# Optimization experiments

Measured on AMD Instinct MI355X. Metric: run time of the kernel, lower is better.

## Reference

```python
import jax, jax.numpy as jnp
import numpy as np
import math

D_MODEL = 1024
NHEAD = 16
D_K = D_MODEL // NHEAD
NUM_LAYERS = 4
D_FF = 4096
SEQ = 2048
BATCH = 1
EPS = 1e-5


def _layer_norm(x, g, b):
    mu = jnp.mean(x, axis=-1, keepdims=True)
    var = jnp.mean((x - mu) ** 2, axis=-1, keepdims=True)
    return (x - mu) * jax.lax.rsqrt(var + EPS) * g + b


def setup_inputs() -> dict:
    key = jax.random.key(0)
    ks = jax.random.split(key, 16)
    s = 0.02
    L, D, F = NUM_LAYERS, D_MODEL, D_FF
    inp = {
        "x": jax.random.normal(ks[0], (BATCH, SEQ, D), dtype=jnp.float32),
        "wq": jax.random.normal(ks[1], (L, D, D), dtype=jnp.float32) * s,
        "bq": jnp.zeros((L, D), dtype=jnp.float32),
        "wk": jax.random.normal(ks[2], (L, D, D), dtype=jnp.float32) * s,
        "bk": jnp.zeros((L, D), dtype=jnp.float32),
        "wv": jax.random.normal(ks[3], (L, D, D), dtype=jnp.float32) * s,
        "bv": jnp.zeros((L, D), dtype=jnp.float32),
        "wo": jax.random.normal(ks[4], (L, D, D), dtype=jnp.float32) * s,
        "bo": jnp.zeros((L, D), dtype=jnp.float32),
        "w1": jax.random.normal(ks[5], (L, D, F), dtype=jnp.float32) * s,
        "b1": jnp.zeros((L, F), dtype=jnp.float32),
        "w2": jax.random.normal(ks[6], (L, F, D), dtype=jnp.float32) * s,
        "b2": jnp.zeros((L, D), dtype=jnp.float32),
        "ln1_g": jnp.ones((L, D), dtype=jnp.float32),
        "ln1_b": jnp.zeros((L, D), dtype=jnp.float32),
        "ln2_g": jnp.ones((L, D), dtype=jnp.float32),
        "ln2_b": jnp.zeros((L, D), dtype=jnp.float32),
    }
    return inp


def _transformer(x, wq, bq, wk, bk, wv, bv, wo, bo, w1, b1, w2, b2,
                 ln1_g, ln1_b, ln2_g, ln2_b):
    B, S, D = x.shape
    scale = math.sqrt(D_K)
    for l in range(NUM_LAYERS):
        # multi-head self-attention (manual QKV matmul + softmax + matmul)
        q = (x @ wq[l] + bq[l]).reshape(B, S, NHEAD, D_K).transpose(0, 2, 1, 3)
        k = (x @ wk[l] + bk[l]).reshape(B, S, NHEAD, D_K).transpose(0, 2, 1, 3)
        v = (x @ wv[l] + bv[l]).reshape(B, S, NHEAD, D_K).transpose(0, 2, 1, 3)
        scores = jnp.einsum('bhqd,bhkd->bhqk', q, k) / scale  # [B,H,S,S]
        attn = jax.nn.softmax(scores, axis=-1)
        ctx = jnp.einsum('bhqk,bhkd->bhqd', attn, v)
        ctx = ctx.transpose(0, 2, 1, 3).reshape(B, S, D)
        attn_out = ctx @ wo[l] + bo[l]
        x = _layer_norm(x + attn_out, ln1_g[l], ln1_b[l])
        # feed-forward network with gelu
        h = jax.nn.gelu(x @ w1[l] + b1[l])
        ffn_out = h @ w2[l] + b2[l]
        x = _layer_norm(x + ffn_out, ln2_g[l], ln2_b[l])
    return x


def reference(x, wq, bq, wk, bk, wv, bv, wo, bo, w1, b1, w2, b2,
              ln1_g, ln1_b, ln2_g, ln2_b):
    return _transformer(x, wq, bq, wk, bk, wv, bv, wo, bo, w1, b1, w2, b2,
                        ln1_g, ln1_b, ln2_g, ln2_b)
```

## Files before the change

kernel.cpp:

```cpp
#include <hip/hip_runtime.h>
#include <hip/hip_bf16.h>
#include <math.h>

typedef __hip_bfloat16 bf16;
typedef __attribute__((ext_vector_type(8))) short bf16x8;
typedef __attribute__((ext_vector_type(4))) short bf16x4;
typedef __attribute__((ext_vector_type(4))) float f32x4;

#define EPI_NONE 0
#define EPI_BIAS_BF16 1
#define EPI_BIAS_GELU_BF16 2

#define CLOG 0.18033688f

__device__ __forceinline__ void gload16(const void* g, void* l) {
  __builtin_amdgcn_global_load_lds((const __attribute__((address_space(1))) void*)g,
                                   (__attribute__((address_space(3))) void*)l, 16, 0, 0);
}

__device__ __forceinline__ float gelu_tanh(float x) {
  const float c = 0.7978845608028654f;
  float t = tanhf(c * (x + 0.044715f * x * x * x));
  return 0.5f * x * (1.0f + t);
}

__device__ __forceinline__ short bf16bits(float x) {
  bf16 h = __float2bfloat16(x);
  return *reinterpret_cast<const short*>(&h);
}

template<int BM, int BN, int BK, int EPI, typename CT>
__global__ __launch_bounds__(256) void gemm_bt(
    const bf16* __restrict__ A, long sAz, int lda,
    const bf16* __restrict__ Bt, long sBz, int ldb,
    CT* __restrict__ C, long sCz, int ldc,
    const float* __restrict__ bias,
    int K, float scale)
{
  constexpr int WM = BM / 2, WN = BN / 2;
  constexpr int MI = WM / 16, NJ = WN / 16;
  constexpr int NA = (BM * BK * 2) / 4096;
  constexpr int NB = (BN * BK * 2) / 4096;
  constexpr int ROWB = BK * 2;
  __shared__ __align__(16) bf16 As[BM * BK];
  __shared__ __align__(16) bf16 Bs[BN * BK];
  const int t = threadIdx.x;
  const int lane = t & 63, w = t >> 6;
  const int wm = (w >> 1) * WM, wn = (w & 1) * WN;
  const int quad = lane >> 4, r16 = lane & 15;
  const long z = blockIdx.z;
  const bf16* Ab = A + z * sAz + (long)blockIdx.y * BM * lda;
  const bf16* Bb = Bt + z * sBz + (long)blockIdx.x * BN * ldb;

  f32x4 acc[MI][NJ];
  #pragma unroll
  for (int i = 0; i < MI; ++i)
    #pragma unroll
    for (int j = 0; j < NJ; ++j)
      acc[i][j] = (f32x4){0.f, 0.f, 0.f, 0.f};

  for (int k0 = 0; k0 < K; k0 += BK) {
    __syncthreads();
    #pragma unroll
    for (int s = 0; s < NA; ++s) {
      int Lb = s * 4096 + t * 16;
      int row = Lb / ROWB, colb = Lb % ROWB;
      gload16((const char*)Ab + (long)row * (lda * 2) + k0 * 2 + colb, (char*)As + Lb);
    }
    #pragma unroll
    for (int s = 0; s < NB; ++s) {
      int Lb = s * 4096 + t * 16;
      int row = Lb / ROWB, colb = Lb % ROWB;
      gload16((const char*)Bb + (long)row * (ldb * 2) + k0 * 2 + colb, (char*)Bs + Lb);
    }
    __syncthreads();

    #pragma unroll
    for (int kk = 0; kk < BK / 32; ++kk) {
      bf16x8 af[MI], bfv[NJ];
      #pragma unroll
      for (int i = 0; i < MI; ++i)
        af[i] = *(const bf16x8*)&As[(wm + i * 16 + r16) * BK + kk * 32 + quad * 8];
      #pragma unroll
      for (int j = 0; j < NJ; ++j)
        bfv[j] = *(const bf16x8*)&Bs[(wn + j * 16 + r16) * BK + kk * 32 + quad * 8];
      #pragma unroll
      for (int i = 0; i < MI; ++i)
        #pragma unroll
        for (int j = 0; j < NJ; ++j)
          acc[i][j] = __builtin_amdgcn_mfma_f32_16x16x32_bf16(af[i], bfv[j], acc[i][j], 0, 0, 0);
    }
  }

  CT* Cb = C + z * sCz;
  #pragma unroll
  for (int i = 0; i < MI; ++i) {
    #pragma unroll
    for (int j = 0; j < NJ; ++j) {
      int col = blockIdx.x * BN + wn + j * 16 + r16;
      float bvv = 0.f;
      if constexpr (EPI == EPI_BIAS_BF16 || EPI == EPI_BIAS_GELU_BF16)
        bvv = bias[col];
      #pragma unroll
      for (int r = 0; r < 4; ++r) {
        long row = (long)blockIdx.y * BM + wm + i * 16 + quad * 4 + r;
        float val = acc[i][j][r] * scale + bvv;
        if constexpr (EPI == EPI_BIAS_GELU_BF16) val = gelu_tanh(val);
        if constexpr (sizeof(CT) == 2)
          Cb[row * (long)ldc + col] = __float2bfloat16(val);
        else
          Cb[row * (long)ldc + col] = val;
      }
    }
  }
}

__global__ __launch_bounds__(256) void flash_attn(
    const bf16* __restrict__ qkv, const bf16* __restrict__ vT,
    float* __restrict__ Osp, float2* __restrict__ ml)
{
  constexpr int SEQ = 2048, LDP = 72, LDPP = 80;
  __shared__ __align__(16) bf16 Qs[64 * 64];
  __shared__ __align__(16) bf16 Ks[64 * LDP];
  __shared__ __align__(16) bf16 VTs[64 * LDP];
  __shared__ __align__(16) bf16 Ps[64 * LDPP];

  const int t = threadIdx.x;
  const int lane = t & 63, w = t >> 6;
  const int quad = lane >> 4, r16 = lane & 15;
  const int wq0 = w * 16;
  const int s0 = blockIdx.x * 64;
  const int h = blockIdx.y;
  const int split = blockIdx.z;
  const int kt0 = split * 16, ktN = kt0 + 16;

  #pragma unroll
  for (int s = 0; s < 2; ++s) {
    int Lb = s * 4096 + t * 16;
    int row = Lb >> 7, colb = Lb & 127;
    int4 v = *(const int4*)(qkv + (long)(s0 + row) * 3072 + h * 64 + (colb >> 1));
    *(int4*)((char*)Qs + Lb) = v;
  }

  const bf16* kp[2]; const bf16* vp[2];
  int krow[2], kcolb[2];
  #pragma unroll
  for (int s = 0; s < 2; ++s) {
    int Lb = s * 4096 + t * 16;
    krow[s] = Lb >> 7; kcolb[s] = Lb & 127;
    kp[s] = qkv + 1024 + (long)h * 64 + (long)krow[s] * 3072 + (kcolb[s] >> 1);
    vp[s] = vT + (long)(h * 64 + krow[s]) * SEQ + (kcolb[s] >> 1);
  }

  int4 rk[2], rv[2];
  #pragma unroll
  for (int s = 0; s < 2; ++s) {
    rk[s] = *(const int4*)(kp[s] + (long)kt0 * 64 * 3072);
    rv[s] = *(const int4*)(vp[s] + (long)kt0 * 64);
  }

  __syncthreads();
  bf16x8 af_q[2];
  #pragma unroll
  for (int kk = 0; kk < 2; ++kk)
    af_q[kk] = *(const bf16x8*)&Qs[(wq0 + r16) * 64 + kk * 32 + quad * 8];

  f32x4 O[4];
  float m_s = -1e30f, l_s = 0.f;
  #pragma unroll
  for (int jd = 0; jd < 4; ++jd) O[jd] = (f32x4){0.f, 0.f, 0.f, 0.f};

  for (int kt = kt0; kt < ktN; ++kt) {
    __syncthreads();
    #pragma unroll
    for (int s = 0; s < 2; ++s) {
      *(int4*)((char*)Ks + (krow[s] * LDP * 2) + kcolb[s]) = rk[s];
      *(int4*)((char*)VTs + (krow[s] * LDP * 2) + kcolb[s]) = rv[s];
    }
    __syncthreads();

    if (kt + 1 < ktN) {
      long k0n = (long)(kt + 1) * 64;
      #pragma unroll
      for (int s = 0; s < 2; ++s) {
        rk[s] = *(const int4*)(kp[s] + k0n * 3072);
        rv[s] = *(const int4*)(vp[s] + k0n);
      }
    }

    f32x4 sc[4];
    #pragma unroll
    for (int j = 0; j < 4; ++j) sc[j] = (f32x4){0.f, 0.f, 0.f, 0.f};
    #pragma unroll
    for (int kk = 0; kk < 2; ++kk) {
      bf16x8 bk_f[4];
      #pragma unroll
      for (int j = 0; j < 4; ++j)
        bk_f[j] = *(const bf16x8*)&Ks[(j * 16 + r16) * LDP + kk * 32 + quad * 8];
      #pragma unroll
      for (int j = 0; j < 4; ++j)
        sc[j] = __builtin_amdgcn_mfma_f32_16x16x32_bf16(bk_f[j], af_q[kk], sc[j], 0, 0, 0);
    }

    float mj[4];
    #pragma unroll
    for (int j = 0; j < 4; ++j)
      mj[j] = fmaxf(fmaxf(sc[j][0], sc[j][1]), fmaxf(sc[j][2], sc[j][3]));
    float mx = fmaxf(fmaxf(mj[0], mj[1]), fmaxf(mj[2], mj[3]));
    mx = fmaxf(mx, __shfl_xor(mx, 16));
    mx = fmaxf(mx, __shfl_xor(mx, 32));
    float m_new = fmaxf(m_s, mx * CLOG);
    float alpha = exp2f(m_s - m_new);
    m_s = m_new;
    float p[4][4], sj[4];
    #pragma unroll
    for (int j = 0; j < 4; ++j) {
      #pragma unroll
      for (int r = 0; r < 4; ++r)
        p[j][r] = exp2f(fmaf(sc[j][r], CLOG, -m_new));
      sj[j] = (p[j][0] + p[j][1]) + (p[j][2] + p[j][3]);
    }
    float rs = (sj[0] + sj[1]) + (sj[2] + sj[3]);
    rs += __shfl_xor(rs, 16);
    rs += __shfl_xor(rs, 32);
    l_s = l_s * alpha + rs;

    float ar[4];
    #pragma unroll
    for (int r = 0; r < 4; ++r)
      ar[r] = __shfl(alpha, quad * 20 + r);
    #pragma unroll
    for (int jd = 0; jd < 4; ++jd)
      #pragma unroll
      for (int r = 0; r < 4; ++r)
        O[jd][r] *= ar[r];

    {
      bf16* pr = &Ps[(wq0 + r16) * LDPP + quad * 4];
      #pragma unroll
      for (int j = 0; j < 4; ++j) {
        bf16x4 pk;
        #pragma unroll
        for (int r = 0; r < 4; ++r)
          pk[r] = bf16bits(p[j][r]);
        *(bf16x4*)(pr + j * 16) = pk;
      }
    }

    #pragma unroll
    for (int kk = 0; kk < 2; ++kk) {
      bf16x8 af_p, bv_f[4];
      af_p = *(const bf16x8*)&Ps[(wq0 + r16) * LDPP + kk * 32 + quad * 8];
      #pragma unroll
      for (int jd = 0; jd < 4; ++jd)
        bv_f[jd] = *(const bf16x8*)&VTs[(jd * 16 + r16) * LDP + kk * 32 + quad * 8];
      #pragma unroll
      for (int jd = 0; jd < 4; ++jd)
        O[jd] = __builtin_amdgcn_mfma_f32_16x16x32_bf16(af_p, bv_f[jd], O[jd], 0, 0, 0);
    }
  }

  float* Ob = Osp + (long)split * SEQ * 1024;
  #pragma unroll
  for (int r = 0; r < 4; ++r) {
    long row = s0 + wq0 + quad * 4 + r;
    #pragma unroll
    for (int jd = 0; jd < 4; ++jd)
      Ob[row * 1024 + h * 64 + jd * 16 + r16] = O[jd][r];
  }
  if (quad == 0)
    ml[((long)(split * 16 + h)) * SEQ + (s0 + wq0 + r16)] = make_float2(m_s, l_s);
}

__global__ __launch_bounds__(256) void attn_combine(
    const float* __restrict__ Osp, const float2* __restrict__ ml,
    bf16* __restrict__ ctx)
{
  constexpr long SD = 2048L * 1024L;
  const int s = blockIdx.x;
  const int t = threadIdx.x;
  #pragma unroll
  for (int i = 0; i < 4; ++i) {
    int c = t + i * 256;
    int h = c >> 6;
    float2 a = ml[(long)h * 2048 + s];
    float2 b = ml[(long)(16 + h) * 2048 + s];
    float mC = fmaxf(a.x, b.x);
    float w0 = exp2f(a.x - mC), w1 = exp2f(b.x - mC);
    float inv = 1.f / (a.y * w0 + b.y * w1);
    float o = (Osp[(long)s * 1024 + c] * w0 + Osp[SD + (long)s * 1024 + c] * w1) * inv;
    ctx[(long)s * 1024 + c] = __float2bfloat16(o);
  }
}

__global__ __launch_bounds__(256) void transpose_cast(
    const float* __restrict__ in, bf16* __restrict__ out, int R, int C)
{
  __shared__ bf16 tile[32][33];
  const int tx = threadIdx.x, ty = threadIdx.y;
  const int r0 = blockIdx.y * 32, c0 = blockIdx.x * 32;
  #pragma unroll
  for (int d = 0; d < 32; d += 8)
    tile[ty + d][tx] = __float2bfloat16(in[(long)(r0 + ty + d) * C + c0 + tx]);
  __syncthreads();
  #pragma unroll
  for (int d = 0; d < 32; d += 8)
    out[(long)(c0 + ty + d) * R + r0 + tx] = tile[tx][ty + d];
}

__global__ __launch_bounds__(256) void transpose_bf16(
    const bf16* __restrict__ in, bf16* __restrict__ out, int R, int C, int ldin)
{
  __shared__ bf16 tile[32][33];
  const int tx = threadIdx.x, ty = threadIdx.y;
  const int r0 = blockIdx.y * 32, c0 = blockIdx.x * 32;
  #pragma unroll
  for (int d = 0; d < 32; d += 8)
    tile[ty + d][tx] = in[(long)(r0 + ty + d) * ldin + c0 + tx];
  __syncthreads();
  #pragma unroll
  for (int d = 0; d < 32; d += 8)
    out[(long)(c0 + ty + d) * R + r0 + tx] = tile[tx][ty + d];
}

__device__ __forceinline__ float blk_sum(float v, float* sh) {
  #pragma unroll
  for (int o = 32; o > 0; o >>= 1) v += __shfl_down(v, o);
  __syncthreads();
  if ((threadIdx.x & 63) == 0) sh[threadIdx.x >> 6] = v;
  __syncthreads();
  return sh[0] + sh[1] + sh[2] + sh[3];
}

__global__ __launch_bounds__(256) void ln_residual2(
    float* __restrict__ X, const float* __restrict__ d0, const float* __restrict__ d1,
    const float* __restrict__ bias,
    const float* __restrict__ g, const float* __restrict__ b,
    bf16* __restrict__ xb)
{
  __shared__ float sh[4];
  const int t = threadIdx.x;
  const long base = (long)blockIdx.x * 1024;
  float v[4]; float s = 0.f;
  #pragma unroll
  for (int i = 0; i < 4; ++i) {
    int c = t + i * 256;
    float val = X[base + c] + d0[base + c] + d1[base + c] + bias[c];
    v[i] = val; s += val;
  }
  s = blk_sum(s, sh);
  const float mu = s * (1.f / 1024.f);
  float s2 = 0.f;
  #pragma unroll
  for (int i = 0; i < 4; ++i) { float d = v[i] - mu; s2 += d * d; }
  s2 = blk_sum(s2, sh);
  const float rs = rsqrtf(s2 * (1.f / 1024.f) + 1e-5f);
  #pragma unroll
  for (int i = 0; i < 4; ++i) {
    int c = t + i * 256;
    float o = (v[i] - mu) * rs * g[c] + b[c];
    X[base + c] = o;
    xb[base + c] = __float2bfloat16(o);
  }
}

__global__ __launch_bounds__(256) void init_x(
    const float* __restrict__ xin, float* __restrict__ X, bf16* __restrict__ xb, int n)
{
  for (int i = blockIdx.x * 256 + threadIdx.x; i < n; i += gridDim.x * 256) {
    float v = xin[i];
    X[i] = v;
    xb[i] = __float2bfloat16(v);
  }
}

__global__ __launch_bounds__(256) void copy_out(
    const float* __restrict__ X, float* __restrict__ out, int n)
{
  for (int i = blockIdx.x * 256 + threadIdx.x; i < n; i += gridDim.x * 256)
    out[i] = X[i];
}

__global__ __launch_bounds__(256) void concat_bias(
    const float* __restrict__ bq, const float* __restrict__ bk,
    const float* __restrict__ bv, float* __restrict__ out, int n)
{
  for (int i = blockIdx.x * 256 + threadIdx.x; i < n; i += gridDim.x * 256) {
    int l = i / 3072, r = i % 3072;
    int j = r / 1024, c = r % 1024;
    const float* src = (j == 0) ? bq : (j == 1) ? bk : bv;
    out[i] = src[l * 1024 + c];
  }
}

extern "C" void kernel_launch(void* const* d_in, const int* in_sizes, int n_in,
                              void* d_out, int out_size, void* d_ws, size_t ws_size,
                              hipStream_t stream) {
  constexpr int S = 2048, D = 1024, F = 4096, L = 4;
  const float* xin = (const float*)d_in[0];
  const float* wq = (const float*)d_in[1];
  const float* bq = (const float*)d_in[2];
  const float* wk = (const float*)d_in[3];
  const float* bk = (const float*)d_in[4];
  const float* wv = (const float*)d_in[5];
  const float* bvp = (const float*)d_in[6];
  const float* wo = (const float*)d_in[7];
  const float* bo = (const float*)d_in[8];
  const float* w1 = (const float*)d_in[9];
  const float* b1 = (const float*)d_in[10];
  const float* w2 = (const float*)d_in[11];
  const float* b2 = (const float*)d_in[12];
  const float* ln1g = (const float*)d_in[13];
  const float* ln1b = (const float*)d_in[14];
  const float* ln2g = (const float*)d_in[15];
  const float* ln2b = (const float*)d_in[16];

  char* p = (char*)d_ws;
  float* X    = (float*)p; p += (long)S * D * 4;
  float* tmpf = (float*)p; p += 2L * S * D * 4;
  bf16* xb    = (bf16*)p;  p += (long)S * D * 2;
  bf16* qkv   = (bf16*)p;
  bf16* hb    = (bf16*)p;  p += (long)S * 3 * D * 2;
  bf16* ctx   = (bf16*)p;  p += (long)S * D * 2;
  bf16* vT    = (bf16*)p;  p += (long)S * D * 2;
  bf16* wT    = (bf16*)p;  p += (long)F * D * 2;
  float* bias3= (float*)p; p += (long)L * 3 * D * 4;
  float2* ml  = (float2*)p; p += 2L * 16 * S * 8;

  init_x<<<2048, 256, 0, stream>>>(xin, X, xb, S * D);
  concat_bias<<<48, 256, 0, stream>>>(bq, bk, bvp, bias3, L * 3 * D);

  for (int l = 0; l < L; ++l) {
    transpose_cast<<<dim3(D / 32, D / 32), dim3(32, 8), 0, stream>>>(wq + (long)l * D * D, wT, D, D);
    transpose_cast<<<dim3(D / 32, D / 32), dim3(32, 8), 0, stream>>>(wk + (long)l * D * D, wT + (long)D * D, D, D);
    transpose_cast<<<dim3(D / 32, D / 32), dim3(32, 8), 0, stream>>>(wv + (long)l * D * D, wT + 2L * D * D, D, D);
    gemm_bt<128, 128, 64, EPI_BIAS_BF16, bf16><<<dim3(3 * D / 128, S / 128, 1), 256, 0, stream>>>(
        xb, 0L, D, wT, 0L, D, qkv, 0L, 3 * D, bias3 + l * 3 * D, D, 1.f);

    transpose_bf16<<<dim3(D / 32, S / 32), dim3(32, 8), 0, stream>>>(qkv + 2 * D, vT, S, D, 3 * D);

    flash_attn<<<dim3(S / 64, 16, 2), 256, 0, stream>>>(qkv, vT, tmpf, ml);
    attn_combine<<<S, 256, 0, stream>>>(tmpf, ml, ctx);

    transpose_cast<<<dim3(D / 32, D / 32), dim3(32, 8), 0, stream>>>(wo + (long)l * D * D, wT, D, D);
    gemm_bt<128, 64, 64, EPI_NONE, float><<<dim3(D / 64, S / 128, 2), 256, 0, stream>>>(
        ctx, (long)(D / 2), D, wT, (long)(D / 2), D, tmpf, (long)S * D, D, nullptr, D / 2, 1.f);
    ln_residual2<<<S, 256, 0, stream>>>(X, tmpf, tmpf + (long)S * D, bo + l * D,
                                        ln1g + l * D, ln1b + l * D, xb);

    transpose_cast<<<dim3(F / 32, D / 32), dim3(32, 8), 0, stream>>>(w1 + (long)l * D * F, wT, D, F);
    gemm_bt<128, 128, 64, EPI_BIAS_GELU_BF16, bf16><<<dim3(F / 128, S / 128, 1), 256, 0, stream>>>(
        xb, 0L, D, wT, 0L, D, hb, 0L, F, b1 + l * F, D, 1.f);
    transpose_cast<<<dim3(D / 32, F / 32), dim3(32, 8), 0, stream>>>(w2 + (long)l * F * D, wT, F, D);
    gemm_bt<128, 64, 64, EPI_NONE, float><<<dim3(D / 64, S / 128, 2), 256, 0, stream>>>(
        hb, (long)(F / 2), F, wT, (long)(F / 2), F, tmpf, (long)S * D, D, nullptr, F / 2, 1.f);
    ln_residual2<<<S, 256, 0, stream>>>(X, tmpf, tmpf + (long)S * D, b2 + l * D,
                                        ln2g + l * D, ln2b + l * D, xb);
  }
  copy_out<<<2048, 256, 0, stream>>>(X, (float*)d_out, S * D);
}
```

Baseline: 1.174 ms.

## Load K/V fragments directly from global memory in flash attention, dropping LDS staging

Each wave now loads its Q, K and V^T MFMA fragments directly from global memory into registers instead of cooperatively staging K and V^T tiles in shared memory. This removes the per-tile LDS writes and both block-wide barriers. It also adds s_setprio around the MFMA bursts and a launch_bounds occupancy hint. In exchange, every one of the four waves now fetches the same K/V tile from global/L2 separately, and the loads sit right before their use without software prefetch, so latency may be exposed.

```diff
diff --git a/kernel.cpp b/kernel.cpp
--- a/kernel.cpp
+++ b/kernel.cpp
@@ -115,14 +115,11 @@
   }
 }
 
-__global__ __launch_bounds__(256) void flash_attn(
+__global__ __launch_bounds__(256, 4) void flash_attn(
     const bf16* __restrict__ qkv, const bf16* __restrict__ vT,
     float* __restrict__ Osp, float2* __restrict__ ml)
 {
-  constexpr int SEQ = 2048, LDP = 72, LDPP = 80;
-  __shared__ __align__(16) bf16 Qs[64 * 64];
-  __shared__ __align__(16) bf16 Ks[64 * LDP];
-  __shared__ __align__(16) bf16 VTs[64 * LDP];
+  constexpr int SEQ = 2048, LDPP = 80;
   __shared__ __align__(16) bf16 Ps[64 * LDPP];
 
   const int t = threadIdx.x;
@@ -134,36 +131,15 @@
   const int split = blockIdx.z;
   const int kt0 = split * 16, ktN = kt0 + 16;
 
-  #pragma unroll
-  for (int s = 0; s < 2; ++s) {
-    int Lb = s * 4096 + t * 16;
-    int row = Lb >> 7, colb = Lb & 127;
-    int4 v = *(const int4*)(qkv + (long)(s0 + row) * 3072 + h * 64 + (colb >> 1));
-    *(int4*)((char*)Qs + Lb) = v;
-  }
-
-  const bf16* kp[2]; const bf16* vp[2];
-  int krow[2], kcolb[2];
-  #pragma unroll
-  for (int s = 0; s < 2; ++s) {
-    int Lb = s * 4096 + t * 16;
-    krow[s] = Lb >> 7; kcolb[s] = Lb & 127;
-    kp[s] = qkv + 1024 + (long)h * 64 + (long)krow[s] * 3072 + (kcolb[s] >> 1);
-    vp[s] = vT + (long)(h * 64 + krow[s]) * SEQ + (kcolb[s] >> 1);
-  }
-
-  int4 rk[2], rv[2];
-  #pragma unroll
-  for (int s = 0; s < 2; ++s) {
-    rk[s] = *(const int4*)(kp[s] + (long)kt0 * 64 * 3072);
-    rv[s] = *(const int4*)(vp[s] + (long)kt0 * 64);
-  }
-
-  __syncthreads();
   bf16x8 af_q[2];
-  #pragma unroll
-  for (int kk = 0; kk < 2; ++kk)
-    af_q[kk] = *(const bf16x8*)&Qs[(wq0 + r16) * 64 + kk * 32 + quad * 8];
+  {
+    const bf16* qp = qkv + (long)(s0 + wq0 + r16) * 3072 + h * 64 + quad * 8;
+    af_q[0] = *(const bf16x8*)(qp);
+    af_q[1] = *(const bf16x8*)(qp + 32);
+  }
+
+  const bf16* kbase = qkv + 1024 + (long)h * 64 + (long)r16 * 3072 + quad * 8;
+  const bf16* vbase = vT + (long)(h * 64 + r16) * SEQ + quad * 8;
 
   f32x4 O[4];
   float m_s = -1e30f, l_s = 0.f;
@@ -171,36 +147,32 @@
   for (int jd = 0; jd < 4; ++jd) O[jd] = (f32x4){0.f, 0.f, 0.f, 0.f};
 
   for (int kt = kt0; kt < ktN; ++kt) {
-    __syncthreads();
-    #pragma unroll
-    for (int s = 0; s < 2; ++s) {
-      *(int4*)((char*)Ks + (krow[s] * LDP * 2) + kcolb[s]) = rk[s];
-      *(int4*)((char*)VTs + (krow[s] * LDP * 2) + kcolb[s]) = rv[s];
-    }
-    __syncthreads();
-
-    if (kt + 1 < ktN) {
-      long k0n = (long)(kt + 1) * 64;
-      #pragma unroll
-      for (int s = 0; s < 2; ++s) {
-        rk[s] = *(const int4*)(kp[s] + k0n * 3072);
-        rv[s] = *(const int4*)(vp[s] + k0n);
-      }
-    }
+    const bf16* kp = kbase + (long)kt * 64 * 3072;
+    bf16x8 bk[2][4];
+    #pragma unroll
+    for (int kk = 0; kk < 2; ++kk)
+      #pragma unroll
+      for (int j = 0; j < 4; ++j)
+        bk[kk][j] = *(const bf16x8*)(kp + (long)j * 16 * 3072 + kk * 32);
 
     f32x4 sc[4];
     #pragma unroll
     for (int j = 0; j < 4; ++j) sc[j] = (f32x4){0.f, 0.f, 0.f, 0.f};
-    #pragma unroll
-    for (int kk = 0; kk < 2; ++kk) {
-      bf16x8 bk_f[4];
+    __builtin_amdgcn_s_setprio(1);
+    #pragma unroll
+    for (int kk = 0; kk < 2; ++kk)
       #pragma unroll
       for (int j = 0; j < 4; ++j)
-        bk_f[j] = *(const bf16x8*)&Ks[(j * 16 + r16) * LDP + kk * 32 + quad * 8];
-      #pragma unroll
-      for (int j = 0; j < 4; ++j)
-        sc[j] = __builtin_amdgcn_mfma_f32_16x16x32_bf16(bk_f[j], af_q[kk], sc[j], 0, 0, 0);
-    }
+        sc[j] = __builtin_amdgcn_mfma_f32_16x16x32_bf16(bk[kk][j], af_q[kk], sc[j], 0, 0, 0);
+    __builtin_amdgcn_s_setprio(0);
+
+    const bf16* vp = vbase + (long)kt * 64;
+    bf16x8 bv[2][4];
+    #pragma unroll
+    for (int kk = 0; kk < 2; ++kk)
+      #pragma unroll
+      for (int jd = 0; jd < 4; ++jd)
+        bv[kk][jd] = *(const bf16x8*)(vp + (long)jd * 16 * SEQ + kk * 32);
 
     float mj[4];
     #pragma unroll
@@ -249,14 +221,12 @@
 
     #pragma unroll
     for (int kk = 0; kk < 2; ++kk) {
-      bf16x8 af_p, bv_f[4];
-      af_p = *(const bf16x8*)&Ps[(wq0 + r16) * LDPP + kk * 32 + quad * 8];
+      bf16x8 af_p = *(const bf16x8*)&Ps[(wq0 + r16) * LDPP + kk * 32 + quad * 8];
+      __builtin_amdgcn_s_setprio(1);
       #pragma unroll
       for (int jd = 0; jd < 4; ++jd)
-        bv_f[jd] = *(const bf16x8*)&VTs[(jd * 16 + r16) * LDP + kk * 32 + quad * 8];
-      #pragma unroll
-      for (int jd = 0; jd < 4; ++jd)
-        O[jd] = __builtin_amdgcn_mfma_f32_16x16x32_bf16(af_p, bv_f[jd], O[jd], 0, 0, 0);
+        O[jd] = __builtin_amdgcn_mfma_f32_16x16x32_bf16(af_p, bv[kk][jd], O[jd], 0, 0, 0);
+      __builtin_amdgcn_s_setprio(0);
     }
   }
 
```

New measurement: 1.314 ms. +11.9%, slower.

## Double-buffer K/V tiles in flash attention with swizzled LDS and fewer barriers

Applied to the files above, without the earlier changes.

Restructures the flash attention inner loop so K and V^T tiles sit in two LDS buffers. The next tile is written after compute, which cuts the loop to one barrier per iteration instead of two. Q fragments now load directly from global memory into registers, dropping the Qs LDS staging. An XOR swizzle is applied to K, V and P LDS addressing to reduce bank conflicts, and s_setprio wraps the MFMA groups. Launch bounds now request 4 blocks per CU, which raises LDS use per block and constrains registers.

```diff
diff --git a/kernel.cpp b/kernel.cpp
--- a/kernel.cpp
+++ b/kernel.cpp
@@ -115,14 +115,15 @@
   }
 }
 
-__global__ __launch_bounds__(256) void flash_attn(
+#define SWZE(row, e) ((e) ^ ((((row) >> 1) & 7) << 3))
+
+__global__ __launch_bounds__(256, 4) void flash_attn(
     const bf16* __restrict__ qkv, const bf16* __restrict__ vT,
     float* __restrict__ Osp, float2* __restrict__ ml)
 {
   constexpr int SEQ = 2048, LDP = 72, LDPP = 80;
-  __shared__ __align__(16) bf16 Qs[64 * 64];
-  __shared__ __align__(16) bf16 Ks[64 * LDP];
-  __shared__ __align__(16) bf16 VTs[64 * LDP];
+  __shared__ __align__(16) bf16 Ks[2][64 * LDP];
+  __shared__ __align__(16) bf16 VTs[2][64 * LDP];
   __shared__ __align__(16) bf16 Ps[64 * LDPP];
 
   const int t = threadIdx.x;
@@ -134,59 +135,62 @@
   const int split = blockIdx.z;
   const int kt0 = split * 16, ktN = kt0 + 16;
 
+  bf16x8 af_q[2];
+  {
+    const bf16* qp = qkv + (long)(s0 + wq0 + r16) * 3072 + h * 64 + quad * 8;
+    af_q[0] = *(const bf16x8*)(qp);
+    af_q[1] = *(const bf16x8*)(qp + 32);
+  }
+
+  const bf16* kp[2]; const bf16* vp[2];
+  int krow[2], kcole[2];
   #pragma unroll
   for (int s = 0; s < 2; ++s) {
     int Lb = s * 4096 + t * 16;
-    int row = Lb >> 7, colb = Lb & 127;
-    int4 v = *(const int4*)(qkv + (long)(s0 + row) * 3072 + h * 64 + (colb >> 1));
-    *(int4*)((char*)Qs + Lb) = v;
-  }
-
-  const bf16* kp[2]; const bf16* vp[2];
-  int krow[2], kcolb[2];
-  #pragma unroll
-  for (int s = 0; s < 2; ++s) {
-    int Lb = s * 4096 + t * 16;
-    krow[s] = Lb >> 7; kcolb[s] = Lb & 127;
-    kp[s] = qkv + 1024 + (long)h * 64 + (long)krow[s] * 3072 + (kcolb[s] >> 1);
-    vp[s] = vT + (long)(h * 64 + krow[s]) * SEQ + (kcolb[s] >> 1);
-  }
-
-  int4 rk[2], rv[2];
-  #pragma unroll
-  for (int s = 0; s < 2; ++s) {
-    rk[s] = *(const int4*)(kp[s] + (long)kt0 * 64 * 3072);
-    rv[s] = *(const int4*)(vp[s] + (long)kt0 * 64);
-  }
-
+    krow[s] = Lb >> 7;
+    int colb = Lb & 127;
+    kcole[s] = colb >> 1;
+    kp[s] = qkv + 1024 + (long)h * 64 + (long)krow[s] * 3072 + kcole[s];
+    vp[s] = vT + (long)(h * 64 + krow[s]) * SEQ + kcole[s];
+  }
+
+  {
+    int4 rk0[2], rv0[2];
+    #pragma unroll
+    for (int s = 0; s < 2; ++s) {
+      rk0[s] = *(const int4*)(kp[s] + (long)kt0 * 64 * 3072);
+      rv0[s] = *(const int4*)(vp[s] + (long)kt0 * 64);
+    }
+    #pragma unroll
+    for (int s = 0; s < 2; ++s) {
+      int e = SWZE(krow[s], krow[s] * LDP + kcole[s]);
+      *(int4*)&Ks[0][e] = rk0[s];
+      *(int4*)&VTs[0][e] = rv0[s];
+    }
+  }
   __syncthreads();
-  bf16x8 af_q[2];
-  #pragma unroll
-  for (int kk = 0; kk < 2; ++kk)
-    af_q[kk] = *(const bf16x8*)&Qs[(wq0 + r16) * 64 + kk * 32 + quad * 8];
 
   f32x4 O[4];
   float m_s = -1e30f, l_s = 0.f;
   #pragma unroll
   for (int jd = 0; jd < 4; ++jd) O[jd] = (f32x4){0.f, 0.f, 0.f, 0.f};
 
+  int cur = 0;
   for (int kt = kt0; kt < ktN; ++kt) {
-    __syncthreads();
-    #pragma unroll
-    for (int s = 0; s < 2; ++s) {
-      *(int4*)((char*)Ks + (krow[s] * LDP * 2) + kcolb[s]) = rk[s];
-      *(int4*)((char*)VTs + (krow[s] * LDP * 2) + kcolb[s]) = rv[s];
-    }
-    __syncthreads();
-
-    if (kt + 1 < ktN) {
+    const bool hasn = (kt + 1 < ktN);
+
+    int4 rkn[2], rvn[2];
+    if (hasn) {
       long k0n = (long)(kt + 1) * 64;
       #pragma unroll
       for (int s = 0; s < 2; ++s) {
-        rk[s] = *(const int4*)(kp[s] + k0n * 3072);
-        rv[s] = *(const int4*)(vp[s] + k0n);
-      }
-    }
+        rkn[s] = *(const int4*)(kp[s] + k0n * 3072);
+        rvn[s] = *(const int4*)(vp[s] + k0n);
+      }
+    }
+
+    const bf16* Kc = Ks[cur];
+    const bf16* Vc = VTs[cur];
 
     f32x4 sc[4];
     #pragma unroll
@@ -195,11 +199,15 @@
     for (int kk = 0; kk < 2; ++kk) {
       bf16x8 bk_f[4];
       #pragma unroll
-      for (int j = 0; j < 4; ++j)
-        bk_f[j] = *(const bf16x8*)&Ks[(j * 16 + r16) * LDP + kk * 32 + quad * 8];
+      for (int j = 0; j < 4; ++j) {
+        int row = j * 16 + r16;
+        bk_f[j] = *(const bf16x8*)&Kc[SWZE(row, row * LDP + kk * 32 + quad * 8)];
+      }
+      __builtin_amdgcn_s_setprio(1);
       #pragma unroll
       for (int j = 0; j < 4; ++j)
         sc[j] = __builtin_amdgcn_mfma_f32_16x16x32_bf16(bk_f[j], af_q[kk], sc[j], 0, 0, 0);
+      __builtin_amdgcn_s_setprio(0);
     }
 
     float mj[4];
@@ -236,27 +244,43 @@
         O[jd][r] *= ar[r];
 
     {
-      bf16* pr = &Ps[(wq0 + r16) * LDPP + quad * 4];
+      int prow = wq0 + r16;
       #pragma unroll
       for (int j = 0; j < 4; ++j) {
         bf16x4 pk;
         #pragma unroll
         for (int r = 0; r < 4; ++r)
           pk[r] = bf16bits(p[j][r]);
-        *(bf16x4*)(pr + j * 16) = pk;
+        *(bf16x4*)&Ps[SWZE(prow, prow * LDPP + j * 16 + quad * 4)] = pk;
       }
     }
 
     #pragma unroll
     for (int kk = 0; kk < 2; ++kk) {
-      bf16x8 af_p, bv_f[4];
-      af_p = *(const bf16x8*)&Ps[(wq0 + r16) * LDPP + kk * 32 + quad * 8];
-      #pragma unroll
-      for (int jd = 0; jd < 4; ++jd)
-        bv_f[jd] = *(const bf16x8*)&VTs[(jd * 16 + r16) * LDP + kk * 32 + quad * 8];
+      int prow = wq0 + r16;
+      bf16x8 af_p = *(const bf16x8*)&Ps[SWZE(prow, prow * LDPP + kk * 32 + quad * 8)];
+      bf16x8 bv_f[4];
+      #pragma unroll
+      for (int jd = 0; jd < 4; ++jd) {
+        int row = jd * 16 + r16;
+        bv_f[jd] = *(const bf16x8*)&Vc[SWZE(row, row * LDP + kk * 32 + quad * 8)];
+      }
+      __builtin_amdgcn_s_setprio(1);
       #pragma unroll
       for (int jd = 0; jd < 4; ++jd)
         O[jd] = __builtin_amdgcn_mfma_f32_16x16x32_bf16(af_p, bv_f[jd], O[jd], 0, 0, 0);
+      __builtin_amdgcn_s_setprio(0);
+    }
+
+    if (hasn) {
+      #pragma unroll
+      for (int s = 0; s < 2; ++s) {
+        int e = SWZE(krow[s], krow[s] * LDP + kcole[s]);
+        *(int4*)&Ks[cur ^ 1][e] = rkn[s];
+        *(int4*)&VTs[cur ^ 1][e] = rvn[s];
+      }
+      __syncthreads();
+      cur ^= 1;
     }
   }
 
```

Result: no change. 1.188 ms (+1.2%).
